# Kernel optimization log

Measured on AMD Instinct MI355X. Metric: run time of the kernel, lower is better.

The kernel has to match this reference:

```python
import jax, jax.numpy as jnp
import numpy as np

E = 1024   # embedding_size
H = 16     # num_heads
DH = E // H


def setup_inputs() -> dict:
    key = jax.random.key(0)
    ks = jax.random.split(key, 11)
    B, S = 2, 2048
    std = 0.02
    return {
        "query": jax.random.normal(ks[0], (B, S, E), jnp.float32),
        "key": jax.random.normal(ks[1], (B, S, E), jnp.float32),
        "value": jax.random.normal(ks[2], (B, S, E), jnp.float32),
        "Wq": jax.random.normal(ks[3], (E, E), jnp.float32) * std,
        "bq": jnp.zeros((E,), jnp.float32),
        "Wk": jax.random.normal(ks[4], (E, E), jnp.float32) * std,
        "bk": jnp.zeros((E,), jnp.float32),
        "Wv": jax.random.normal(ks[5], (E, E), jnp.float32) * std,
        "bv": jnp.zeros((E,), jnp.float32),
        "Wo": jax.random.normal(ks[6], (E, E), jnp.float32) * std,
        "bo": jnp.zeros((E,), jnp.float32),
    }


def _split_heads(x, B, S):
    # [B,S,E] -> [B,H,S,DH]
    return x.reshape(B, S, H, DH).transpose(0, 2, 1, 3)


def reference(query, key, value, Wq, bq, Wk, bk, Wv, bv, Wo, bo):
    B, S, _ = query.shape
    # torch Linear: y = x @ W.T + b
    q = _split_heads(query @ Wq.T + bq, B, S)
    k = _split_heads(key @ Wk.T + bk, B, key.shape[1])
    v = _split_heads(value @ Wv.T + bv, B, value.shape[1])
    # naive unscaled attention (original has no 1/sqrt(d) factor)
    scores = jnp.einsum("bhsd,bhtd->bhst", q, k)  # [B,H,S,T]
    attn = jax.nn.softmax(scores, axis=-1)
    out = jnp.einsum("bhst,bhtd->bhsd", attn, v)  # [B,H,S,DH]
    out = out.transpose(0, 2, 1, 3).reshape(B, S, E)
    return out @ Wo.T + bo
```

## Files before the change

kernel.cpp:

```cpp
#include <hip/hip_runtime.h>
#include <hip/hip_bf16.h>

constexpr int kB   = 2;
constexpr int kS   = 2048;
constexpr int kE   = 1024;
constexpr int kH   = 16;
constexpr int kDH  = 64;
constexpr int kTok = kB * kS;

constexpr float kLog2e = 1.4426950408889634f;

typedef short bf16x8 __attribute__((ext_vector_type(8)));
typedef float f32x4  __attribute__((ext_vector_type(4)));
typedef unsigned int uint2v __attribute__((ext_vector_type(2)));

__device__ __forceinline__ float bf2f(unsigned short s) {
  union { unsigned int u; float f; } c; c.u = ((unsigned int)s) << 16; return c.f;
}
__device__ __forceinline__ unsigned short f2bf(float f) {
  union { float f; unsigned int u; } c; c.f = f;
  unsigned int u = c.u;
  u += 0x7fffu + ((u >> 16) & 1u);
  return (unsigned short)(u >> 16);
}

__device__ __forceinline__ unsigned cvtpk(float lo, float hi) {
  unsigned r;
  asm("v_cvt_pk_bf16_f32 %0, %1, %2" : "=v"(r) : "v"(lo), "v"(hi));
  return r;
}

__device__ __forceinline__ float fexp2(float x) {
  float r;
  asm("v_exp_f32 %0, %1" : "=v"(r) : "v"(x));
  return r;
}

__device__ __forceinline__ void gl_lds16(const unsigned short* g, unsigned short* l) {
  __builtin_amdgcn_global_load_lds(
      (const __attribute__((address_space(1))) unsigned int*)g,
      (__attribute__((address_space(3))) unsigned int*)l, 16, 0, 0);
}

__global__ void detect_dtype(const unsigned short* __restrict__ q, int* flag) {
  __shared__ int cnt;
  if (threadIdx.x == 0) cnt = 0;
  __syncthreads();
  int bad = 0;
  for (int i = threadIdx.x; i < 4096; i += 256) {
    unsigned int e = (q[i] >> 7) & 0xFF;
    if (e >= 0xC0) bad++;
  }
  atomicAdd(&cnt, bad);
  __syncthreads();
  if (threadIdx.x == 0) *flag = (cnt > 8) ? 1 : 0;
}

struct Seg { const void* src; unsigned short* dst; unsigned int n; unsigned int blk0; };
struct ConvArgs { Seg s[11]; float scale[11]; };

__global__ __launch_bounds__(256) void conv_all(ConvArgs a, const int* __restrict__ flag) {
  const unsigned int bid = blockIdx.x;
  int si = 0;
  #pragma unroll
  for (int i = 1; i < 11; ++i)
    if (bid >= a.s[i].blk0) si = i;
  const Seg sg = a.s[si];
  const float sc = a.scale[si];
  const int i0 = ((int)(bid - sg.blk0) * 256 + threadIdx.x) * 8;
  if (i0 >= (int)sg.n) return;
  if (*flag) {
    const float* s = (const float*)sg.src + i0;
    f32x4 f0 = *(const f32x4*)(s);
    f32x4 f1 = *(const f32x4*)(s + 4);
    bf16x8 v;
    #pragma unroll
    for (int j = 0; j < 4; ++j) v[j]     = (short)f2bf(f0[j] * sc);
    #pragma unroll
    for (int j = 0; j < 4; ++j) v[j + 4] = (short)f2bf(f1[j] * sc);
    *(bf16x8*)&sg.dst[i0] = v;
  } else {
    bf16x8 v = *(const bf16x8*)((const unsigned short*)sg.src + i0);
    if (sc != 1.0f) {
      #pragma unroll
      for (int j = 0; j < 8; ++j)
        v[j] = (short)f2bf(bf2f((unsigned short)v[j]) * sc);
    }
    *(bf16x8*)&sg.dst[i0] = v;
  }
}

__device__ __forceinline__ void gemm_core(
    const unsigned short* __restrict__ A,
    const unsigned short* __restrict__ W,
    int Kdim, int bM, int bN,
    unsigned short* As, unsigned short* Ws,
    f32x4 acc[4][4])
{
  const int tid  = threadIdx.x;
  const int lane = tid & 63;
  const int wv   = tid >> 6;
  const int wm   = (wv >> 1) * 64;
  const int wn   = (wv & 1) * 64;
  const int lr   = lane & 15;
  const int kq   = (lane >> 4) * 8;

  const int r0 = tid >> 2;
  const int c0 = (tid & 3) * 8;

  const unsigned short* Ag = A + (size_t)(bM + r0) * Kdim + c0;
  const unsigned short* Wg = W + (size_t)(bN + r0) * Kdim + c0;
  unsigned short* lA = &As[tid * 8];
  unsigned short* lW = &Ws[tid * 8];

  gl_lds16(Ag,                      lA);
  gl_lds16(Ag + (size_t)64 * Kdim,  lA + 2048);
  gl_lds16(Wg,                      lW);
  gl_lds16(Wg + (size_t)64 * Kdim,  lW + 2048);
  __syncthreads();

  for (int k0 = 0; k0 < Kdim; k0 += 32) {
    const int co = ((k0 >> 5) & 1) * 4096;
    if (k0 + 32 < Kdim) {
      const int no = co ^ 4096;
      gl_lds16(Ag + k0 + 32,                      lA + no);
      gl_lds16(Ag + (size_t)64 * Kdim + k0 + 32,  lA + no + 2048);
      gl_lds16(Wg + k0 + 32,                      lW + no);
      gl_lds16(Wg + (size_t)64 * Kdim + k0 + 32,  lW + no + 2048);
    }

    bf16x8 a[4], b[4];
    #pragma unroll
    for (int i = 0; i < 4; ++i)
      a[i] = *(const bf16x8*)&As[co + (wm + i * 16 + lr) * 32 + kq];
    #pragma unroll
    for (int i = 0; i < 4; ++i)
      b[i] = *(const bf16x8*)&Ws[co + (wn + i * 16 + lr) * 32 + kq];
    #pragma unroll
    for (int i = 0; i < 4; ++i)
      #pragma unroll
      for (int j = 0; j < 4; ++j)
        acc[i][j] = __builtin_amdgcn_mfma_f32_16x16x32_bf16(a[i], b[j], acc[i][j], 0, 0, 0);

    __syncthreads();
  }
}

__global__ __launch_bounds__(256) void gemm_qkv(
    const unsigned short* __restrict__ Abase,
    const unsigned short* __restrict__ Wbase,
    const unsigned short* __restrict__ biasbase,
    unsigned short* __restrict__ Cbase)
{
  __shared__ unsigned short As[2 * 128 * 32];
  __shared__ unsigned short Ws[2 * 128 * 32];

  const int bid = blockIdx.x + (blockIdx.y << 3) + (blockIdx.z << 8);
  const int swz = (bid & 7) * 96 + (bid >> 3);
  const int z   = swz >> 8;
  const int rem = swz & 255;
  const int bM  = (rem >> 3) * 128;
  const int bN  = (rem & 7) * 128;

  const unsigned short* A    = Abase    + (size_t)z * (kTok * kE);
  const unsigned short* W    = Wbase    + (size_t)z * (kE * kE);
  const unsigned short* bias = biasbase + (size_t)z * kE;
  unsigned short* C          = Cbase    + (size_t)z * (kTok * kE);

  f32x4 acc[4][4] = {};
  gemm_core(A, W, kE, bM, bN, As, Ws, acc);

  const int lane = threadIdx.x & 63;
  const int wv   = threadIdx.x >> 6;
  const int wm   = (wv >> 1) * 64;
  const int wn   = (wv & 1) * 64;
  const int lr   = lane & 15;
  const int qd   = lane >> 4;
  #pragma unroll
  for (int j = 0; j < 4; ++j) {
    const int col = bN + wn + j * 16 + lr;
    const float bb = bf2f(bias[col]);
    #pragma unroll
    for (int i = 0; i < 4; ++i)
      #pragma unroll
      for (int r = 0; r < 4; ++r) {
        const int row = bM + wm + i * 16 + qd * 4 + r;
        C[(size_t)row * kE + col] = f2bf(acc[i][j][r] + bb);
      }
  }
}

__global__ __launch_bounds__(256) void vtrans(
    const unsigned short* __restrict__ Vb,
    unsigned short* __restrict__ Vt)
{
  __shared__ unsigned short Lt[64 * 72];
  const int tid = threadIdx.x;
  const int bh  = blockIdx.y;
  const int b   = bh >> 4;
  const int h   = bh & 15;
  const int hcol = h * kDH;
  const int s0  = blockIdx.x * 64;

  #pragma unroll
  for (int issue = 0; issue < 2; ++issue) {
    int g = issue * 256 + tid;
    int r = g >> 3, c = (g & 7) * 8;
    bf16x8 vv = *(const bf16x8*)&Vb[(size_t)(b * kS + s0 + r) * kE + hcol + c];
    const int swz = ((((r >> 3) ^ (c >> 3)) & 7) << 3) + (r & 7);
    #pragma unroll
    for (int i = 0; i < 8; ++i)
      Lt[(c + i) * 72 + swz] = (unsigned short)vv[i];
  }
  __syncthreads();
  #pragma unroll
  for (int issue = 0; issue < 2; ++issue) {
    int g = issue * 256 + tid;
    int f = g >> 3, tc = (g & 7) * 8;
    const int blk = ((tc >> 3) ^ (f >> 3)) & 7;
    bf16x8 vv = *(const bf16x8*)&Lt[f * 72 + (blk << 3)];
    *(bf16x8*)&Vt[(size_t)b * (kE * kS) + (size_t)(hcol + f) * kS + s0 + tc] = vv;
  }
}

__global__ __launch_bounds__(256) void gemm_out(
    const unsigned short* __restrict__ A,
    const unsigned short* __restrict__ W,
    const unsigned short* __restrict__ bias,
    void* __restrict__ C,
    const int* __restrict__ flag)
{
  __shared__ unsigned short As[2 * 128 * 32];
  __shared__ unsigned short Ws[2 * 128 * 32];

  const int bid = blockIdx.x + (blockIdx.y << 3);
  const int swz = (bid & 7) * 32 + (bid >> 3);
  const int bM  = (swz >> 3) * 128;
  const int bN  = (swz & 7) * 128;

  f32x4 acc[4][4] = {};
  gemm_core(A, W, kE, bM, bN, As, Ws, acc);

  const int lane = threadIdx.x & 63;
  const int wv   = threadIdx.x >> 6;
  const int wm   = (wv >> 1) * 64;
  const int wn   = (wv & 1) * 64;
  const int lr   = lane & 15;
  const int qd   = lane >> 4;
  if (*flag) {
    float* Cf = (float*)C;
    #pragma unroll
    for (int j = 0; j < 4; ++j) {
      const int col = bN + wn + j * 16 + lr;
      const float bb = bf2f(bias[col]);
      #pragma unroll
      for (int i = 0; i < 4; ++i)
        #pragma unroll
        for (int r = 0; r < 4; ++r) {
          const int row = bM + wm + i * 16 + qd * 4 + r;
          Cf[(size_t)row * kE + col] = acc[i][j][r] + bb;
        }
    }
  } else {
    unsigned short* Cb = (unsigned short*)C;
    #pragma unroll
    for (int j = 0; j < 4; ++j) {
      const int col = bN + wn + j * 16 + lr;
      const float bb = bf2f(bias[col]);
      #pragma unroll
      for (int i = 0; i < 4; ++i)
        #pragma unroll
        for (int r = 0; r < 4; ++r) {
          const int row = bM + wm + i * 16 + qd * 4 + r;
          Cb[(size_t)row * kE + col] = f2bf(acc[i][j][r] + bb);
        }
    }
  }
}

__global__ __launch_bounds__(256) void attn(
    const unsigned short* __restrict__ Qb,
    const unsigned short* __restrict__ Kb,
    const unsigned short* __restrict__ Vt,
    unsigned short* __restrict__ Ob)
{
  __shared__ unsigned short Ks[2][64 * 72];
  __shared__ unsigned short Vs[2][64 * 72];

  const int tid  = threadIdx.x;
  const int lane = tid & 63;
  const int w    = tid >> 6;
  const int lr   = lane & 15;
  const int quad = lane >> 4;
  const int kq   = quad * 8;

  const int bid = blockIdx.x + (blockIdx.y << 4);
  const int swz = (bid & 7) * 64 + (bid >> 3);
  const int bh  = swz >> 4;
  const int b   = bh >> 4;
  const int h   = bh & 15;
  const int q0  = (swz & 15) * 128;

  const size_t rowbase = (size_t)b * kS * kE;
  const int hcol = h * kDH;
  const unsigned short* Vbase = Vt + (size_t)b * (kE * kS) + (size_t)hcol * kS;

  const int r0 = tid >> 3;
  const int c0 = (tid & 7) * 8;

  bf16x8 aq[2][2];
  #pragma unroll
  for (int rg = 0; rg < 2; ++rg)
    #pragma unroll
    for (int hh = 0; hh < 2; ++hh)
      aq[rg][hh] = *(const bf16x8*)
          &Qb[rowbase + (size_t)(q0 + w * 32 + rg * 16 + lr) * kE + hcol + hh * 32 + kq];

  f32x4 o[2][4] = {};
  float l4[2][4] = {};

  bf16x8 rk0 = *(const bf16x8*)&Kb[rowbase + (size_t)(r0)      * kE + hcol + c0];
  bf16x8 rk1 = *(const bf16x8*)&Kb[rowbase + (size_t)(r0 + 32) * kE + hcol + c0];
  bf16x8 rv0 = *(const bf16x8*)&Vbase[(size_t)(r0)      * kS + c0];
  bf16x8 rv1 = *(const bf16x8*)&Vbase[(size_t)(r0 + 32) * kS + c0];
  *(bf16x8*)&Ks[0][ r0       * 72 + c0] = rk0;
  *(bf16x8*)&Ks[0][(r0 + 32) * 72 + c0] = rk1;
  *(bf16x8*)&Vs[0][ r0       * 72 + c0] = rv0;
  *(bf16x8*)&Vs[0][(r0 + 32) * 72 + c0] = rv1;
  rk0 = *(const bf16x8*)&Kb[rowbase + (size_t)(64 + r0)      * kE + hcol + c0];
  rk1 = *(const bf16x8*)&Kb[rowbase + (size_t)(64 + r0 + 32) * kE + hcol + c0];
  rv0 = *(const bf16x8*)&Vbase[(size_t)(r0)      * kS + 64 + c0];
  rv1 = *(const bf16x8*)&Vbase[(size_t)(r0 + 32) * kS + 64 + c0];
  __syncthreads();

  for (int t0 = 0; t0 < kS; t0 += 64) {
    const int cur = (t0 >> 6) & 1;
    const int nxt = cur ^ 1;

    if (t0 + 64 < kS) {
      *(bf16x8*)&Ks[nxt][ r0       * 72 + c0] = rk0;
      *(bf16x8*)&Ks[nxt][(r0 + 32) * 72 + c0] = rk1;
      *(bf16x8*)&Vs[nxt][ r0       * 72 + c0] = rv0;
      *(bf16x8*)&Vs[nxt][(r0 + 32) * 72 + c0] = rv1;
    }
    if (t0 + 128 < kS) {
      const int t2 = t0 + 128;
      rk0 = *(const bf16x8*)&Kb[rowbase + (size_t)(t2 + r0)      * kE + hcol + c0];
      rk1 = *(const bf16x8*)&Kb[rowbase + (size_t)(t2 + r0 + 32) * kE + hcol + c0];
      rv0 = *(const bf16x8*)&Vbase[(size_t)(r0)      * kS + t2 + c0];
      rv1 = *(const bf16x8*)&Vbase[(size_t)(r0 + 32) * kS + t2 + c0];
    }

    f32x4 s[2][4];
    #pragma unroll
    for (int rg = 0; rg < 2; ++rg)
      #pragma unroll
      for (int tn = 0; tn < 4; ++tn)
        s[rg][tn] = f32x4{0.f, 0.f, 0.f, 0.f};
    __builtin_amdgcn_s_setprio(1);
    #pragma unroll
    for (int tn = 0; tn < 4; ++tn) {
      const bf16x8 bk0 = *(const bf16x8*)&Ks[cur][(tn * 16 + lr) * 72 + 0 + kq];
      const bf16x8 bk1 = *(const bf16x8*)&Ks[cur][(tn * 16 + lr) * 72 + 32 + kq];
      #pragma unroll
      for (int rg = 0; rg < 2; ++rg) {
        s[rg][tn] = __builtin_amdgcn_mfma_f32_16x16x32_bf16(bk0, aq[rg][0], s[rg][tn], 0, 0, 0);
        s[rg][tn] = __builtin_amdgcn_mfma_f32_16x16x32_bf16(bk1, aq[rg][1], s[rg][tn], 0, 0, 0);
      }
    }
    __builtin_amdgcn_s_setprio(0);

    #pragma unroll
    for (int rg = 0; rg < 2; ++rg)
      #pragma unroll
      for (int tn = 0; tn < 4; ++tn)
        #pragma unroll
        for (int r = 0; r < 4; ++r) {
          const float e = fexp2(s[rg][tn][r]);
          s[rg][tn][r] = e;
          l4[rg][r] += e;
        }

    bf16x8 ap[2][2];
    #pragma unroll
    for (int rg = 0; rg < 2; ++rg)
      #pragma unroll
      for (int kk = 0; kk < 2; ++kk) {
        const unsigned A0 = cvtpk(s[rg][2 * kk][0],     s[rg][2 * kk][1]);
        const unsigned A1 = cvtpk(s[rg][2 * kk + 1][0], s[rg][2 * kk + 1][1]);
        const uint2v u   = __builtin_amdgcn_permlane32_swap(A0, A1, false, false);
        const uint2v z02 = __builtin_amdgcn_permlane16_swap(u[0], u[1], false, false);
        const unsigned B0 = cvtpk(s[rg][2 * kk][2],     s[rg][2 * kk][3]);
        const unsigned B1 = cvtpk(s[rg][2 * kk + 1][2], s[rg][2 * kk + 1][3]);
        const uint2v v2  = __builtin_amdgcn_permlane32_swap(B0, B1, false, false);
        const uint2v z13 = __builtin_amdgcn_permlane16_swap(v2[0], v2[1], false, false);
        union { unsigned ud[4]; bf16x8 v; } pk;
        pk.ud[0] = z02[0];
        pk.ud[1] = z13[0];
        pk.ud[2] = z02[1];
        pk.ud[3] = z13[1];
        ap[rg][kk] = pk.v;
      }

    __builtin_amdgcn_s_setprio(1);
    #pragma unroll
    for (int kk = 0; kk < 2; ++kk)
      #pragma unroll
      for (int dt = 0; dt < 4; ++dt) {
        const bf16x8 bv = *(const bf16x8*)&Vs[cur][(dt * 16 + lr) * 72 + kk * 32 + kq];
        #pragma unroll
        for (int rg = 0; rg < 2; ++rg)
          o[rg][dt] = __builtin_amdgcn_mfma_f32_16x16x32_bf16(ap[rg][kk], bv, o[rg][dt], 0, 0, 0);
      }
    __builtin_amdgcn_s_setprio(0);

    __syncthreads();
  }

  #pragma unroll
  for (int rg = 0; rg < 2; ++rg) {
    float l = (l4[rg][0] + l4[rg][1]) + (l4[rg][2] + l4[rg][3]);
    l += __shfl_xor(l, 16, 64);
    l += __shfl_xor(l, 32, 64);
    float inv[4];
    #pragma unroll
    for (int r = 0; r < 4; ++r)
      inv[r] = 1.0f / __shfl(l, quad * 4 + r, 64);

    #pragma unroll
    for (int dt = 0; dt < 4; ++dt) {
      #pragma unroll
      for (int r = 0; r < 4; ++r) {
        const int row = q0 + w * 32 + rg * 16 + quad * 4 + r;
        const int col = hcol + dt * 16 + lr;
        Ob[rowbase + (size_t)row * kE + col] = f2bf(o[rg][dt][r] * inv[r]);
      }
    }
  }
}

extern "C" void kernel_launch(void* const* d_in, const int* in_sizes, int n_in,
                              void* d_out, int out_size, void* d_ws, size_t ws_size,
                              hipStream_t stream) {
  const int nQKV = kTok * kE;
  const int nW   = kE * kE;
  const int nB   = kE;

  char* wsb = (char*)d_ws;
  int* flag = (int*)wsb;
  unsigned short* qc  = (unsigned short*)(wsb + 16);
  unsigned short* kc  = qc  + (size_t)nQKV;
  unsigned short* vc  = kc  + (size_t)nQKV;
  unsigned short* Wqc = vc  + (size_t)nQKV;
  unsigned short* Wkc = Wqc + (size_t)nW;
  unsigned short* Wvc = Wkc + (size_t)nW;
  unsigned short* Woc = Wvc + (size_t)nW;
  unsigned short* bqc = Woc + (size_t)nW;
  unsigned short* bkc = bqc + nB;
  unsigned short* bvc = bkc + nB;
  unsigned short* boc = bvc + nB;
  unsigned short* Qb  = boc + nB;
  unsigned short* Kb  = Qb  + (size_t)nQKV;
  unsigned short* Vb  = Kb  + (size_t)nQKV;
  unsigned short* Vtb = kc;
  unsigned short* Ob  = qc;

  detect_dtype<<<1, 256, 0, stream>>>((const unsigned short*)d_in[0], flag);

  ConvArgs ca;
  const void* srcs[11] = { d_in[0], d_in[1], d_in[2], d_in[3], d_in[4], d_in[5],
                           d_in[6], d_in[7], d_in[8], d_in[9], d_in[10] };
  unsigned short* dsts[11] = { qc, kc, vc, Wqc, bqc, Wkc, bkc, Wvc, bvc, Woc, boc };
  const unsigned int ns[11] = { (unsigned)nQKV, (unsigned)nQKV, (unsigned)nQKV,
                                (unsigned)nW, (unsigned)nB, (unsigned)nW, (unsigned)nB,
                                (unsigned)nW, (unsigned)nB, (unsigned)nW, (unsigned)nB };
  unsigned int blk = 0;
  for (int i = 0; i < 11; ++i) {
    ca.s[i].src = srcs[i]; ca.s[i].dst = dsts[i]; ca.s[i].n = ns[i]; ca.s[i].blk0 = blk;
    ca.scale[i] = 1.0f;
    blk += (ns[i] + 2047) / 2048;
  }
  ca.scale[3] = kLog2e;
  ca.scale[4] = kLog2e;
  conv_all<<<blk, 256, 0, stream>>>(ca, flag);

  dim3 blk256(256);
  dim3 gqkv(kE / 128, kTok / 128, 3);
  gemm_qkv<<<gqkv, blk256, 0, stream>>>(qc, Wqc, bqc, Qb);

  dim3 gvt(kS / 64, kB * kH);
  vtrans<<<gvt, blk256, 0, stream>>>(Vb, Vtb);

  dim3 gattn(kS / 128, kB * kH);
  attn<<<gattn, blk256, 0, stream>>>(Qb, Kb, Vtb, Ob);

  dim3 gout(kE / 128, kTok / 128);
  gemm_out<<<gout, blk256, 0, stream>>>(Ob, Woc, boc, d_out, flag);
}
```

Measured before the change: 248.6 us.

## Software-pipeline attention loop so PV matmul of previous tile overlaps softmax

Restructures the attention main loop so each iteration computes QK^T for the current key tile, then the P·V product for the previous tile, then the exp/pack of the current scores. The V shared-memory buffer becomes triple-buffered so the previous tile's V stays valid while the next one is written. The loop is unrolled by two with ping-pong register arrays for the packed probabilities, plus an epilogue for the last tile. The aim is to let MFMA work overlap the transcendental and permute work. The cost is extra registers and LDS, which could lower occupancy.

Result: no change. 249.5 us (+0.3%).

```diff
diff --git a/kernel.cpp b/kernel.cpp
--- a/kernel.cpp
+++ b/kernel.cpp
@@ -285,7 +285,7 @@
     unsigned short* __restrict__ Ob)
 {
   __shared__ unsigned short Ks[2][64 * 72];
-  __shared__ unsigned short Vs[2][64 * 72];
+  __shared__ unsigned short Vs[3][64 * 72];
 
   const int tid  = threadIdx.x;
   const int lane = tid & 63;
@@ -333,24 +333,26 @@
   rv1 = *(const bf16x8*)&Vbase[(size_t)(r0 + 32) * kS + 64 + c0];
   __syncthreads();
 
-  for (int t0 = 0; t0 < kS; t0 += 64) {
-    const int cur = (t0 >> 6) & 1;
-    const int nxt = cur ^ 1;
-
-    if (t0 + 64 < kS) {
-      *(bf16x8*)&Ks[nxt][ r0       * 72 + c0] = rk0;
-      *(bf16x8*)&Ks[nxt][(r0 + 32) * 72 + c0] = rk1;
-      *(bf16x8*)&Vs[nxt][ r0       * 72 + c0] = rv0;
-      *(bf16x8*)&Vs[nxt][(r0 + 32) * 72 + c0] = rv1;
-    }
-    if (t0 + 128 < kS) {
-      const int t2 = t0 + 128;
+  bf16x8 apA[2][2], apB[2][2];
+
+  auto body = [&](int t, bf16x8 (&apW)[2][2], bf16x8 (&apR)[2][2]) {
+    if (t < 31) {
+      const int kn = (t + 1) & 1;
+      const int vn = (t + 1) % 3;
+      *(bf16x8*)&Ks[kn][ r0       * 72 + c0] = rk0;
+      *(bf16x8*)&Ks[kn][(r0 + 32) * 72 + c0] = rk1;
+      *(bf16x8*)&Vs[vn][ r0       * 72 + c0] = rv0;
+      *(bf16x8*)&Vs[vn][(r0 + 32) * 72 + c0] = rv1;
+    }
+    if (t + 2 < 32) {
+      const int t2 = (t + 2) * 64;
       rk0 = *(const bf16x8*)&Kb[rowbase + (size_t)(t2 + r0)      * kE + hcol + c0];
       rk1 = *(const bf16x8*)&Kb[rowbase + (size_t)(t2 + r0 + 32) * kE + hcol + c0];
       rv0 = *(const bf16x8*)&Vbase[(size_t)(r0)      * kS + t2 + c0];
       rv1 = *(const bf16x8*)&Vbase[(size_t)(r0 + 32) * kS + t2 + c0];
     }
 
+    const int kc = t & 1;
     f32x4 s[2][4];
     #pragma unroll
     for (int rg = 0; rg < 2; ++rg)
@@ -360,8 +362,8 @@
     __builtin_amdgcn_s_setprio(1);
     #pragma unroll
     for (int tn = 0; tn < 4; ++tn) {
-      const bf16x8 bk0 = *(const bf16x8*)&Ks[cur][(tn * 16 + lr) * 72 + 0 + kq];
-      const bf16x8 bk1 = *(const bf16x8*)&Ks[cur][(tn * 16 + lr) * 72 + 32 + kq];
+      const bf16x8 bk0 = *(const bf16x8*)&Ks[kc][(tn * 16 + lr) * 72 + 0 + kq];
+      const bf16x8 bk1 = *(const bf16x8*)&Ks[kc][(tn * 16 + lr) * 72 + 32 + kq];
       #pragma unroll
       for (int rg = 0; rg < 2; ++rg) {
         s[rg][tn] = __builtin_amdgcn_mfma_f32_16x16x32_bf16(bk0, aq[rg][0], s[rg][tn], 0, 0, 0);
@@ -369,6 +371,21 @@
       }
     }
     __builtin_amdgcn_s_setprio(0);
+
+    if (t > 0) {
+      const int vp = (t - 1) % 3;
+      __builtin_amdgcn_s_setprio(1);
+      #pragma unroll
+      for (int kk = 0; kk < 2; ++kk)
+        #pragma unroll
+        for (int dt = 0; dt < 4; ++dt) {
+          const bf16x8 bv = *(const bf16x8*)&Vs[vp][(dt * 16 + lr) * 72 + kk * 32 + kq];
+          #pragma unroll
+          for (int rg = 0; rg < 2; ++rg)
+            o[rg][dt] = __builtin_amdgcn_mfma_f32_16x16x32_bf16(apR[rg][kk], bv, o[rg][dt], 0, 0, 0);
+        }
+      __builtin_amdgcn_s_setprio(0);
+    }
 
     #pragma unroll
     for (int rg = 0; rg < 2; ++rg)
@@ -381,7 +398,6 @@
           l4[rg][r] += e;
         }
 
-    bf16x8 ap[2][2];
     #pragma unroll
     for (int rg = 0; rg < 2; ++rg)
       #pragma unroll
@@ -399,22 +415,29 @@
         pk.ud[1] = z13[0];
         pk.ud[2] = z02[1];
         pk.ud[3] = z13[1];
-        ap[rg][kk] = pk.v;
+        apW[rg][kk] = pk.v;
       }
-
+  };
+
+  for (int tt = 0; tt < 32; tt += 2) {
+    body(tt,     apA, apB);
+    __syncthreads();
+    body(tt + 1, apB, apA);
+    __syncthreads();
+  }
+
+  {
     __builtin_amdgcn_s_setprio(1);
     #pragma unroll
     for (int kk = 0; kk < 2; ++kk)
       #pragma unroll
       for (int dt = 0; dt < 4; ++dt) {
-        const bf16x8 bv = *(const bf16x8*)&Vs[cur][(dt * 16 + lr) * 72 + kk * 32 + kq];
+        const bf16x8 bv = *(const bf16x8*)&Vs[1][(dt * 16 + lr) * 72 + kk * 32 + kq];
         #pragma unroll
         for (int rg = 0; rg < 2; ++rg)
-          o[rg][dt] = __builtin_amdgcn_mfma_f32_16x16x32_bf16(ap[rg][kk], bv, o[rg][dt], 0, 0, 0);
+          o[rg][dt] = __builtin_amdgcn_mfma_f32_16x16x32_bf16(apB[rg][kk], bv, o[rg][dt], 0, 0, 0);
       }
     __builtin_amdgcn_s_setprio(0);
-
-    __syncthreads();
   }
 
   #pragma unroll
```

## Halve attention query tile per block and compute row sums via MFMA with ones

Applied to the files above, without the earlier changes.

Each attention block now handles 64 query rows instead of 128 (16 per wave), which doubles the grid to 1024 blocks and halves per-thread accumulator registers. The softmax denominator is no longer accumulated with scalar adds and cross-lane shuffles. It is instead produced by an extra MFMA of the bf16 probabilities against a vector of ones. The trade-offs are that K/V tiles are loaded twice as often in total, and the row sums now come from bf16-rounded probabilities rather than fp32 ones.

New measurement: 256.5 us. 3.2% more time.

```diff
diff --git a/kernel.cpp b/kernel.cpp
--- a/kernel.cpp
+++ b/kernel.cpp
@@ -294,12 +294,12 @@
   const int quad = lane >> 4;
   const int kq   = quad * 8;
 
-  const int bid = blockIdx.x + (blockIdx.y << 4);
-  const int swz = (bid & 7) * 64 + (bid >> 3);
-  const int bh  = swz >> 4;
+  const int bid = blockIdx.x + (blockIdx.y << 5);
+  const int swz = (bid & 7) * 128 + (bid >> 3);
+  const int bh  = swz >> 5;
   const int b   = bh >> 4;
   const int h   = bh & 15;
-  const int q0  = (swz & 15) * 128;
+  const int q0  = (swz & 31) * 64;
 
   const size_t rowbase = (size_t)b * kS * kE;
   const int hcol = h * kDH;
@@ -308,16 +308,18 @@
   const int r0 = tid >> 3;
   const int c0 = (tid & 7) * 8;
 
-  bf16x8 aq[2][2];
-  #pragma unroll
-  for (int rg = 0; rg < 2; ++rg)
-    #pragma unroll
-    for (int hh = 0; hh < 2; ++hh)
-      aq[rg][hh] = *(const bf16x8*)
-          &Qb[rowbase + (size_t)(q0 + w * 32 + rg * 16 + lr) * kE + hcol + hh * 32 + kq];
-
-  f32x4 o[2][4] = {};
-  float l4[2][4] = {};
+  bf16x8 aq[2];
+  #pragma unroll
+  for (int hh = 0; hh < 2; ++hh)
+    aq[hh] = *(const bf16x8*)
+        &Qb[rowbase + (size_t)(q0 + w * 16 + lr) * kE + hcol + hh * 32 + kq];
+
+  bf16x8 ones;
+  #pragma unroll
+  for (int j = 0; j < 8; ++j) ones[j] = (short)0x3F80;
+
+  f32x4 o[4] = {};
+  f32x4 ol   = {};
 
   bf16x8 rk0 = *(const bf16x8*)&Kb[rowbase + (size_t)(r0)      * kE + hcol + c0];
   bf16x8 rk1 = *(const bf16x8*)&Kb[rowbase + (size_t)(r0 + 32) * kE + hcol + c0];
@@ -351,90 +353,72 @@
       rv1 = *(const bf16x8*)&Vbase[(size_t)(r0 + 32) * kS + t2 + c0];
     }
 
-    f32x4 s[2][4];
-    #pragma unroll
-    for (int rg = 0; rg < 2; ++rg)
-      #pragma unroll
-      for (int tn = 0; tn < 4; ++tn)
-        s[rg][tn] = f32x4{0.f, 0.f, 0.f, 0.f};
+    f32x4 s[4];
+    #pragma unroll
+    for (int tn = 0; tn < 4; ++tn)
+      s[tn] = f32x4{0.f, 0.f, 0.f, 0.f};
     __builtin_amdgcn_s_setprio(1);
     #pragma unroll
     for (int tn = 0; tn < 4; ++tn) {
       const bf16x8 bk0 = *(const bf16x8*)&Ks[cur][(tn * 16 + lr) * 72 + 0 + kq];
       const bf16x8 bk1 = *(const bf16x8*)&Ks[cur][(tn * 16 + lr) * 72 + 32 + kq];
-      #pragma unroll
-      for (int rg = 0; rg < 2; ++rg) {
-        s[rg][tn] = __builtin_amdgcn_mfma_f32_16x16x32_bf16(bk0, aq[rg][0], s[rg][tn], 0, 0, 0);
-        s[rg][tn] = __builtin_amdgcn_mfma_f32_16x16x32_bf16(bk1, aq[rg][1], s[rg][tn], 0, 0, 0);
-      }
+      s[tn] = __builtin_amdgcn_mfma_f32_16x16x32_bf16(bk0, aq[0], s[tn], 0, 0, 0);
+      s[tn] = __builtin_amdgcn_mfma_f32_16x16x32_bf16(bk1, aq[1], s[tn], 0, 0, 0);
     }
     __builtin_amdgcn_s_setprio(0);
 
     #pragma unroll
-    for (int rg = 0; rg < 2; ++rg)
-      #pragma unroll
-      for (int tn = 0; tn < 4; ++tn)
-        #pragma unroll
-        for (int r = 0; r < 4; ++r) {
-          const float e = fexp2(s[rg][tn][r]);
-          s[rg][tn][r] = e;
-          l4[rg][r] += e;
-        }
-
-    bf16x8 ap[2][2];
-    #pragma unroll
-    for (int rg = 0; rg < 2; ++rg)
-      #pragma unroll
-      for (int kk = 0; kk < 2; ++kk) {
-        const unsigned A0 = cvtpk(s[rg][2 * kk][0],     s[rg][2 * kk][1]);
-        const unsigned A1 = cvtpk(s[rg][2 * kk + 1][0], s[rg][2 * kk + 1][1]);
-        const uint2v u   = __builtin_amdgcn_permlane32_swap(A0, A1, false, false);
-        const uint2v z02 = __builtin_amdgcn_permlane16_swap(u[0], u[1], false, false);
-        const unsigned B0 = cvtpk(s[rg][2 * kk][2],     s[rg][2 * kk][3]);
-        const unsigned B1 = cvtpk(s[rg][2 * kk + 1][2], s[rg][2 * kk + 1][3]);
-        const uint2v v2  = __builtin_amdgcn_permlane32_swap(B0, B1, false, false);
-        const uint2v z13 = __builtin_amdgcn_permlane16_swap(v2[0], v2[1], false, false);
-        union { unsigned ud[4]; bf16x8 v; } pk;
-        pk.ud[0] = z02[0];
-        pk.ud[1] = z13[0];
-        pk.ud[2] = z02[1];
-        pk.ud[3] = z13[1];
-        ap[rg][kk] = pk.v;
-      }
+    for (int tn = 0; tn < 4; ++tn)
+      #pragma unroll
+      for (int r = 0; r < 4; ++r)
+        s[tn][r] = fexp2(s[tn][r]);
+
+    bf16x8 ap[2];
+    #pragma unroll
+    for (int kk = 0; kk < 2; ++kk) {
+      const unsigned A0 = cvtpk(s[2 * kk][0],     s[2 * kk][1]);
+      const unsigned A1 = cvtpk(s[2 * kk + 1][0], s[2 * kk + 1][1]);
+      const uint2v u   = __builtin_amdgcn_permlane32_swap(A0, A1, false, false);
+      const uint2v z02 = __builtin_amdgcn_permlane16_swap(u[0], u[1], false, false);
+      const unsigned B0 = cvtpk(s[2 * kk][2],     s[2 * kk][3]);
+      const unsigned B1 = cvtpk(s[2 * kk + 1][2], s[2 * kk + 1][3]);
+      const uint2v v2  = __builtin_amdgcn_permlane32_swap(B0, B1, false, false);
+      const uint2v z13 = __builtin_amdgcn_permlane16_swap(v2[0], v2[1], false, false);
+      union { unsigned ud[4]; bf16x8 v; } pk;
+      pk.ud[0] = z02[0];
+      pk.ud[1] = z13[0];
+      pk.ud[2] = z02[1];
+      pk.ud[3] = z13[1];
+      ap[kk] = pk.v;
+    }
 
     __builtin_amdgcn_s_setprio(1);
     #pragma unroll
-    for (int kk = 0; kk < 2; ++kk)
+    for (int kk = 0; kk < 2; ++kk) {
       #pragma unroll
       for (int dt = 0; dt < 4; ++dt) {
         const bf16x8 bv = *(const bf16x8*)&Vs[cur][(dt * 16 + lr) * 72 + kk * 32 + kq];
-        #pragma unroll
-        for (int rg = 0; rg < 2; ++rg)
-          o[rg][dt] = __builtin_amdgcn_mfma_f32_16x16x32_bf16(ap[rg][kk], bv, o[rg][dt], 0, 0, 0);
+        o[dt] = __builtin_amdgcn_mfma_f32_16x16x32_bf16(ap[kk], bv, o[dt], 0, 0, 0);
       }
+      ol = __builtin_amdgcn_mfma_f32_16x16x32_bf16(ap[kk], ones, ol, 0, 0, 0);
+    }
     __builtin_amdgcn_s_setprio(0);
 
     __syncthreads();
   }
 
-  #pragma unroll
-  for (int rg = 0; rg < 2; ++rg) {
-    float l = (l4[rg][0] + l4[rg][1]) + (l4[rg][2] + l4[rg][3]);
-    l += __shfl_xor(l, 16, 64);
-    l += __shfl_xor(l, 32, 64);
-    float inv[4];
-    #pragma unroll
-    for (int r = 0; r < 4; ++r)
-      inv[r] = 1.0f / __shfl(l, quad * 4 + r, 64);
-
-    #pragma unroll
-    for (int dt = 0; dt < 4; ++dt) {
-      #pragma unroll
-      for (int r = 0; r < 4; ++r) {
-        const int row = q0 + w * 32 + rg * 16 + quad * 4 + r;
-        const int col = hcol + dt * 16 + lr;
-        Ob[rowbase + (size_t)row * kE + col] = f2bf(o[rg][dt][r] * inv[r]);
-      }
+  float inv[4];
+  #pragma unroll
+  for (int r = 0; r < 4; ++r)
+    inv[r] = 1.0f / ol[r];
+
+  #pragma unroll
+  for (int dt = 0; dt < 4; ++dt) {
+    #pragma unroll
+    for (int r = 0; r < 4; ++r) {
+      const int row = q0 + w * 16 + quad * 4 + r;
+      const int col = hcol + dt * 16 + lr;
+      Ob[rowbase + (size_t)row * kE + col] = f2bf(o[dt][r] * inv[r]);
     }
   }
 }
@@ -491,7 +475,7 @@
   dim3 gvt(kS / 64, kB * kH);
   vtrans<<<gvt, blk256, 0, stream>>>(Vb, Vtb);
 
-  dim3 gattn(kS / 128, kB * kH);
+  dim3 gattn(kS / 64, kB * kH);
   attn<<<gattn, blk256, 0, stream>>>(Qb, Kb, Vtb, Ob);
 
   dim3 gout(kE / 128, kTok / 128);
```

## Use 64-wide K tiles in output GEMM and MFMA-based softmax row sums

Applied to the files above, without the earlier changes.

Adds a gemm_core64 path that stages 64-wide K slices with direct global-to-LDS loads, halving the number of K iterations and barriers in the output projection, at the cost of doubled LDS per block. In attention, the softmax denominator is now computed by an extra MFMA of the bf16 probabilities against a vector of ones, replacing per-element scalar accumulation and the final cross-lane shuffles. The denominator now sums bf16-rounded probabilities, which matches the numerator's rounding but adds MFMA work per tile.

After: 245.9 us. No clear change (-1.1%).

```diff
diff --git a/kernel.cpp b/kernel.cpp
--- a/kernel.cpp
+++ b/kernel.cpp
@@ -146,6 +146,65 @@
   }
 }
 
+__device__ __forceinline__ void gemm_core64(
+    const unsigned short* __restrict__ A,
+    const unsigned short* __restrict__ W,
+    int Kdim, int bM, int bN,
+    unsigned short* As, unsigned short* Ws,
+    f32x4 acc[4][4])
+{
+  const int tid  = threadIdx.x;
+  const int lane = tid & 63;
+  const int wv   = tid >> 6;
+  const int wm   = (wv >> 1) * 64;
+  const int wn   = (wv & 1) * 64;
+  const int lr   = lane & 15;
+  const int kq   = (lane >> 4) * 8;
+
+  const int r0 = tid >> 3;
+  const int c0 = (tid & 7) * 8;
+
+  const unsigned short* Ag = A + (size_t)(bM + r0) * Kdim + c0;
+  const unsigned short* Wg = W + (size_t)(bN + r0) * Kdim + c0;
+  unsigned short* lA = &As[tid * 8];
+  unsigned short* lW = &Ws[tid * 8];
+
+  #pragma unroll
+  for (int j = 0; j < 4; ++j) {
+    gl_lds16(Ag + (size_t)(32 * j) * Kdim, lA + j * 2048);
+    gl_lds16(Wg + (size_t)(32 * j) * Kdim, lW + j * 2048);
+  }
+  __syncthreads();
+
+  for (int k0 = 0; k0 < Kdim; k0 += 64) {
+    const int co = ((k0 >> 6) & 1) * 8192;
+    if (k0 + 64 < Kdim) {
+      const int no = co ^ 8192;
+      #pragma unroll
+      for (int j = 0; j < 4; ++j) {
+        gl_lds16(Ag + (size_t)(32 * j) * Kdim + k0 + 64, lA + no + j * 2048);
+        gl_lds16(Wg + (size_t)(32 * j) * Kdim + k0 + 64, lW + no + j * 2048);
+      }
+    }
+    #pragma unroll
+    for (int kk2 = 0; kk2 < 2; ++kk2) {
+      bf16x8 a[4], b[4];
+      #pragma unroll
+      for (int i = 0; i < 4; ++i)
+        a[i] = *(const bf16x8*)&As[co + (wm + i * 16 + lr) * 64 + kk2 * 32 + kq];
+      #pragma unroll
+      for (int i = 0; i < 4; ++i)
+        b[i] = *(const bf16x8*)&Ws[co + (wn + i * 16 + lr) * 64 + kk2 * 32 + kq];
+      #pragma unroll
+      for (int i = 0; i < 4; ++i)
+        #pragma unroll
+        for (int j = 0; j < 4; ++j)
+          acc[i][j] = __builtin_amdgcn_mfma_f32_16x16x32_bf16(a[i], b[j], acc[i][j], 0, 0, 0);
+    }
+    __syncthreads();
+  }
+}
+
 __global__ __launch_bounds__(256) void gemm_qkv(
     const unsigned short* __restrict__ Abase,
     const unsigned short* __restrict__ Wbase,
@@ -230,8 +289,8 @@
     void* __restrict__ C,
     const int* __restrict__ flag)
 {
-  __shared__ unsigned short As[2 * 128 * 32];
-  __shared__ unsigned short Ws[2 * 128 * 32];
+  __shared__ unsigned short As[2 * 128 * 64];
+  __shared__ unsigned short Ws[2 * 128 * 64];
 
   const int bid = blockIdx.x + (blockIdx.y << 3);
   const int swz = (bid & 7) * 32 + (bid >> 3);
@@ -239,7 +298,7 @@
   const int bN  = (swz & 7) * 128;
 
   f32x4 acc[4][4] = {};
-  gemm_core(A, W, kE, bM, bN, As, Ws, acc);
+  gemm_core64(A, W, kE, bM, bN, As, Ws, acc);
 
   const int lane = threadIdx.x & 63;
   const int wv   = threadIdx.x >> 6;
@@ -316,8 +375,12 @@
       aq[rg][hh] = *(const bf16x8*)
           &Qb[rowbase + (size_t)(q0 + w * 32 + rg * 16 + lr) * kE + hcol + hh * 32 + kq];
 
+  bf16x8 ones;
+  #pragma unroll
+  for (int j = 0; j < 8; ++j) ones[j] = (short)0x3F80;
+
   f32x4 o[2][4] = {};
-  float l4[2][4] = {};
+  f32x4 ol[2]   = {};
 
   bf16x8 rk0 = *(const bf16x8*)&Kb[rowbase + (size_t)(r0)      * kE + hcol + c0];
   bf16x8 rk1 = *(const bf16x8*)&Kb[rowbase + (size_t)(r0 + 32) * kE + hcol + c0];
@@ -375,11 +438,8 @@
       #pragma unroll
       for (int tn = 0; tn < 4; ++tn)
         #pragma unroll
-        for (int r = 0; r < 4; ++r) {
-          const float e = fexp2(s[rg][tn][r]);
-          s[rg][tn][r] = e;
-          l4[rg][r] += e;
-        }
+        for (int r = 0; r < 4; ++r)
+          s[rg][tn][r] = fexp2(s[rg][tn][r]);
 
     bf16x8 ap[2][2];
     #pragma unroll
@@ -404,7 +464,7 @@
 
     __builtin_amdgcn_s_setprio(1);
     #pragma unroll
-    for (int kk = 0; kk < 2; ++kk)
+    for (int kk = 0; kk < 2; ++kk) {
       #pragma unroll
       for (int dt = 0; dt < 4; ++dt) {
         const bf16x8 bv = *(const bf16x8*)&Vs[cur][(dt * 16 + lr) * 72 + kk * 32 + kq];
@@ -412,6 +472,10 @@
         for (int rg = 0; rg < 2; ++rg)
           o[rg][dt] = __builtin_amdgcn_mfma_f32_16x16x32_bf16(ap[rg][kk], bv, o[rg][dt], 0, 0, 0);
       }
+      #pragma unroll
+      for (int rg = 0; rg < 2; ++rg)
+        ol[rg] = __builtin_amdgcn_mfma_f32_16x16x32_bf16(ap[rg][kk], ones, ol[rg], 0, 0, 0);
+    }
     __builtin_amdgcn_s_setprio(0);
 
     __syncthreads();
@@ -419,13 +483,10 @@
 
   #pragma unroll
   for (int rg = 0; rg < 2; ++rg) {
-    float l = (l4[rg][0] + l4[rg][1]) + (l4[rg][2] + l4[rg][3]);
-    l += __shfl_xor(l, 16, 64);
-    l += __shfl_xor(l, 32, 64);
     float inv[4];
     #pragma unroll
     for (int r = 0; r < 4; ++r)
-      inv[r] = 1.0f / __shfl(l, quad * 4 + r, 64);
+      inv[r] = 1.0f / ol[rg][r];
 
     #pragma unroll
     for (int dt = 0; dt < 4; ++dt) {
```
